# Kernel optimization log

Measured on AMD Instinct MI355X. Metric: run time of the kernel, lower is better.

Reference implementation:

```python
import jax, jax.numpy as jnp
import numpy as np

GROUPS = 32
EPS = 1e-5


def group_norm(x, gamma, beta):
    # x: [N, C, H, W]
    N, C, H, W = x.shape
    xg = x.reshape(N, GROUPS, C // GROUPS, H, W)
    mean = xg.mean(axis=(2, 3, 4), keepdims=True)
    var = xg.var(axis=(2, 3, 4), keepdims=True)
    xg = (xg - mean) * jax.lax.rsqrt(var + EPS)
    x = xg.reshape(N, C, H, W)
    return x * gamma[None, :, None, None] + beta[None, :, None, None]


def conv1x1(x, w, b):
    # x: [N, C, H, W], w: [O, C], b: [O]
    return jnp.einsum('nchw,oc->nohw', x, w) + b[None, :, None, None]


def setup_inputs() -> dict:
    key = jax.random.key(0)
    ks = jax.random.split(key, 12)
    N, C, H, W = 16, 512, 32, 32
    s = 1.0 / np.sqrt(C)
    inp = {
        'x': jax.random.normal(ks[0], (N, C, H, W), dtype=jnp.float32),
        'gamma': jnp.ones((C,), dtype=jnp.float32),
        'beta': jnp.zeros((C,), dtype=jnp.float32),
        'wq': jax.random.normal(ks[1], (C, C), dtype=jnp.float32) * s,
        'bq': jnp.zeros((C,), dtype=jnp.float32),
        'wk': jax.random.normal(ks[2], (C, C), dtype=jnp.float32) * s,
        'bk': jnp.zeros((C,), dtype=jnp.float32),
        'wv': jax.random.normal(ks[3], (C, C), dtype=jnp.float32) * s,
        'bv': jnp.zeros((C,), dtype=jnp.float32),
        'wo': jax.random.normal(ks[4], (C, C), dtype=jnp.float32) * s,
        'bo': jnp.zeros((C,), dtype=jnp.float32),
    }
    return inp


def reference(x, gamma, beta, wq, bq, wk, bk, wv, bv, wo, bo):
    N, C, H, W = x.shape
    h = group_norm(x, gamma, beta)
    q = conv1x1(h, wq, bq)  # [N, C, H, W]
    k = conv1x1(h, wk, bk)
    v = conv1x1(h, wv, bv)
    # flatten spatial dims to sequence of length S = H*W
    q = q.reshape(N, C, H * W).transpose(0, 2, 1)  # [N, S, C]
    k = k.reshape(N, C, H * W)                     # [N, C, S]
    v = v.reshape(N, C, H * W).transpose(0, 2, 1)  # [N, S, C]
    scale = C ** (-0.5)
    w = jnp.einsum('nsc,nct->nst', q, k) * scale   # [N, S, S]
    w = jax.nn.softmax(w, axis=-1)
    h = jnp.einsum('nst,ntc->nsc', w, v)           # [N, S, C]
    h = h.reshape(N, H, W, C).transpose(0, 3, 1, 2)  # [N, C, H, W]
    h = conv1x1(h, wo, bo)
    return x + h
```

## Files before the change

### kernel.cpp

```cpp
#include <hip/hip_runtime.h>

#define GROUPS 32
#define EPS 1e-5f

typedef unsigned short u16;
typedef __bf16 bf16x8 __attribute__((ext_vector_type(8)));
typedef float f32x4 __attribute__((ext_vector_type(4)));

__device__ __forceinline__ u16 f2bf(float f) {
  unsigned x = __builtin_bit_cast(unsigned, f);
  x += 0x7FFFu + ((x >> 16) & 1u);
  return (u16)(x >> 16);
}
__device__ __forceinline__ float bf2f(u16 u) {
  unsigned x = ((unsigned)u) << 16;
  return __builtin_bit_cast(float, x);
}

__device__ __forceinline__ void gload_lds16(const void* g, void* l) {
  __builtin_amdgcn_global_load_lds(
      (const __attribute__((address_space(1))) void*)g,
      (__attribute__((address_space(3))) void*)l, 16, 0, 0);
}

__global__ __launch_bounds__(256) void prep_kernel(
    const float* __restrict__ x, const float* __restrict__ gamma,
    const float* __restrict__ beta, u16* __restrict__ HT,
    const float* __restrict__ wq, const float* __restrict__ wk,
    const float* __restrict__ wv, const float* __restrict__ wo,
    const float* __restrict__ bq, const float* __restrict__ bk,
    u16* __restrict__ Wqk, u16* __restrict__ Wv, u16* __restrict__ Wo,
    float* __restrict__ bqk, float* __restrict__ lsum,
    int C, int S, int CC, int NG) {
  __shared__ float xs[16 * 1024];
  __shared__ float rs[4], rss[4];
  int b = blockIdx.x;
  int tid = threadIdx.x;

  if (b >= NG) {
    int cb = b - NG;
    if (cb < 1024) {
      int w = cb >> 8, blk = cb & 255;
      const float* src;
      u16* dst;
      switch (w) {
        case 0: src = wq; dst = Wqk; break;
        case 1: src = wk; dst = Wqk + CC; break;
        case 2: src = wv; dst = Wv; break;
        default: src = wo; dst = Wo; break;
      }
      int i = (blk * 256 + tid) * 4;
      float4 v = *(const float4*)&src[i];
      ushort4 o;
      o.x = f2bf(v.x); o.y = f2bf(v.y); o.z = f2bf(v.z); o.w = f2bf(v.w);
      *(ushort4*)&dst[i] = o;
    } else if (cb < 1028) {
      int j = (cb - 1024) * 256 + tid;
      if (j < C) bqk[j] = bq[j];
      else if (j < 2 * C) bqk[j] = bk[j - C];
    } else {
      int i = (cb - 1028) * 1024 + tid * 4;
      *(float4*)&lsum[i] = make_float4(0.f, 0.f, 0.f, 0.f);
    }
    return;
  }

  const int cpg = C / GROUPS;
  int n = b / GROUPS;
  int g = b % GROUPS;
  const float* xb = x + ((size_t)n * C + (size_t)g * cpg) * S;
  int cnt = cpg * S;
  float s = 0.f, ss = 0.f;
  for (int i = tid * 4; i < cnt; i += 256 * 4) {
    float4 v = *(const float4*)&xb[i];
    *(float4*)&xs[i] = v;
    s += v.x + v.y + v.z + v.w;
    ss += v.x * v.x + v.y * v.y + v.z * v.z + v.w * v.w;
  }
  for (int o = 32; o > 0; o >>= 1) {
    s += __shfl_xor(s, o);
    ss += __shfl_xor(ss, o);
  }
  int wave = tid >> 6, lane = tid & 63;
  if (lane == 0) { rs[wave] = s; rss[wave] = ss; }
  __syncthreads();
  float S1 = rs[0] + rs[1] + rs[2] + rs[3];
  float S2 = rss[0] + rss[1] + rss[2] + rss[3];
  float mean = S1 / (float)cnt;
  float var = S2 / (float)cnt - mean * mean;
  float rstd = rsqrtf(var + EPS);
  float gm[16], bt[16];
#pragma unroll
  for (int c = 0; c < 16; ++c) {
    float gmv = gamma[g * cpg + c] * rstd;
    gm[c] = gmv;
    bt[c] = beta[g * cpg + c] - mean * gmv;
  }
  for (int i = 0; i < S; i += 256) {
    int sp = i + tid;
    u16 outv[16];
#pragma unroll
    for (int c = 0; c < 16; ++c) {
      float h = xs[c * 1024 + sp] * gm[c] + bt[c];
      outv[c] = f2bf(h);
    }
    u16* dst = HT + ((size_t)n * S + sp) * C + g * cpg;
    *(int4*)dst = *(int4*)&outv[0];
    *(int4*)&dst[8] = *(int4*)&outv[8];
  }
}

__device__ __forceinline__ void gemm_body(
    int bid, int nblk,
    const u16* __restrict__ A, long lda, long strideA,
    const u16* __restrict__ B, long ldb, long strideB,
    void* __restrict__ Out, long ldo, long strideO, int out_fp32,
    const float* __restrict__ bias, int bias_mode,
    float scale, const float* __restrict__ residual, int K,
    int nbx, int nby, u16* lds, int epi_mode, float* epi_ptr) {
  u16* As0 = lds;
  u16* Bs0 = lds + 8192;
  u16* As1 = lds + 12288;
  u16* Bs1 = lds + 20480;

  int tid = threadIdx.x;
  int wave = tid >> 6, lane = tid & 63;
  int wr = wave >> 1, wc = wave & 1;
  int l15 = lane & 15, l4 = lane >> 4;

  int tilesPB = nbx * nby;
  int nz = nblk / tilesPB;
  int z, rem;
  if ((nz & 7) == 0) {
    int e = bid & 7, j = bid >> 3;
    z = e + 8 * (j / tilesPB);
    rem = j % tilesPB;
  } else {
    int swz = ((nblk & 7) == 0) ? (bid & 7) * (nblk >> 3) + (bid >> 3) : bid;
    z = swz / tilesPB; rem = swz % tilesPB;
  }
  int bx = rem % nbx, by = rem / nbx;

  const u16* Ab = A + (long)z * strideA + (long)by * 256 * lda;
  const u16* Bb = B + (long)z * strideB + (long)bx * 128 * ldb;

  auto STAGE = [&](u16* Ad, u16* Bd, int kt) {
#pragma unroll
    for (int i = 0; i < 2; ++i) {
      int c = i * 512 + tid;
      int l = c >> 3, p = c & 7;
      int q = p ^ (l & 7);
      int row = 2 * l + (q >> 2);
      long koff = (long)kt * 32 + (q & 3) * 8;
      int lbase = (i * 512 + wave * 64) * 8;
      gload_lds16(Ab + (long)row * lda + koff, Ad + lbase);
    }
    {
      int c = tid;
      int l = c >> 3, p = c & 7;
      int q = p ^ (l & 7);
      int row = 2 * l + (q >> 2);
      long koff = (long)kt * 32 + (q & 3) * 8;
      int lbase = (wave * 64) * 8;
      gload_lds16(Bb + (long)row * ldb + koff, Bd + lbase);
    }
  };

  f32x4 acc[4][4] = {};

  auto COMPUTE = [&](const u16* Asrc, const u16* Bsrc) {
    bf16x8 af[4], bfr[4];
#pragma unroll
    for (int m = 0; m < 4; ++m) {
      int R = wr * 64 + m * 16 + l15;
      int line = R >> 1;
      int p = ((R & 1) * 4 + l4) ^ (line & 7);
      af[m] = *(const bf16x8*)&Asrc[line * 64 + p * 8];
    }
#pragma unroll
    for (int n = 0; n < 4; ++n) {
      int R = wc * 64 + n * 16 + l15;
      int line = R >> 1;
      int p = ((R & 1) * 4 + l4) ^ (line & 7);
      bfr[n] = *(const bf16x8*)&Bsrc[line * 64 + p * 8];
    }
#pragma unroll
    for (int m = 0; m < 4; ++m)
#pragma unroll
      for (int n = 0; n < 4; ++n)
        acc[m][n] = __builtin_amdgcn_mfma_f32_16x16x32_bf16(
            af[m], bfr[n], acc[m][n], 0, 0, 0);
  };

  int NT = K >> 5;
  u16 *Ar = As0, *Br = Bs0, *Aw = As1, *Bw = Bs1;

  STAGE(Ar, Br, 0);
  asm volatile("s_waitcnt vmcnt(0)" ::: "memory");
  __builtin_amdgcn_sched_barrier(0);
  __builtin_amdgcn_s_barrier();
  __builtin_amdgcn_sched_barrier(0);

  for (int t = 0; t < NT - 1; ++t) {
    STAGE(Aw, Bw, t + 1);
    COMPUTE(Ar, Br);
    asm volatile("s_waitcnt vmcnt(0)" ::: "memory");
    __builtin_amdgcn_sched_barrier(0);
    __builtin_amdgcn_s_barrier();
    __builtin_amdgcn_sched_barrier(0);
    u16* tp;
    tp = Ar; Ar = Aw; Aw = tp;
    tp = Br; Br = Bw; Bw = tp;
  }
  COMPUTE(Ar, Br);

  long orow0 = (long)by * 256 + wr * 64;
  long ocol0 = (long)bx * 128 + wc * 64;
  long rows_pb = 256L * nby;
  long cols_pb = 128L * nbx;

  float inv4[4];
  if (epi_mode == 2) {
#pragma unroll
    for (int n = 0; n < 4; ++n)
      inv4[n] = 1.f / epi_ptr[z * cols_pb + ocol0 + n * 16 + l15];
  }
  float rowpart[4][4];
  if (epi_mode == 1) {
#pragma unroll
    for (int m = 0; m < 4; ++m)
#pragma unroll
      for (int r = 0; r < 4; ++r) rowpart[m][r] = 0.f;
  }

#pragma unroll
  for (int m = 0; m < 4; ++m) {
#pragma unroll
    for (int n = 0; n < 4; ++n) {
#pragma unroll
      for (int r = 0; r < 4; ++r) {
        long row = orow0 + m * 16 + l4 * 4 + r;
        long col = ocol0 + n * 16 + l15;
        long off = (long)z * strideO + row * ldo + col;
        float v = acc[m][n][r] * scale;
        if (epi_mode == 1) {
          u16 e = f2bf(__expf(v));
          ((u16*)Out)[off] = e;
          rowpart[m][r] += bf2f(e);
        } else {
          if (epi_mode == 2) v *= inv4[n];
          if (bias_mode == 1) v += bias[row];
          else if (bias_mode == 2) v += bias[col];
          if (residual) v += residual[off];
          if (out_fp32) ((float*)Out)[off] = v;
          else ((u16*)Out)[off] = f2bf(v);
        }
      }
    }
  }

  if (epi_mode == 1) {
#pragma unroll
    for (int m = 0; m < 4; ++m)
#pragma unroll
      for (int r = 0; r < 4; ++r) {
        float t = rowpart[m][r];
        t += __shfl_xor(t, 1);
        t += __shfl_xor(t, 2);
        t += __shfl_xor(t, 4);
        t += __shfl_xor(t, 8);
        if (l15 == 0) {
          long row = orow0 + m * 16 + l4 * 4 + r;
          atomicAdd(&epi_ptr[z * rows_pb + row], t);
        }
      }
  }
}

__global__ __launch_bounds__(512, 4) void gemm256x128_kernel(
    const u16* __restrict__ A, long lda, long strideA,
    const u16* __restrict__ B, long ldb, long strideB,
    void* __restrict__ Out, long ldo, long strideO, int out_fp32,
    const float* __restrict__ bias, int bias_mode,
    float scale, const float* __restrict__ residual, int K, int nbx, int nby,
    int epi_mode, float* epi_ptr) {
  __shared__ u16 lds[24576];
  gemm_body(blockIdx.x, gridDim.x, A, lda, strideA, B, ldb, strideB,
            Out, ldo, strideO, out_fp32, bias, bias_mode, scale, residual,
            K, nbx, nby, lds, epi_mode, epi_ptr);
}

__global__ __launch_bounds__(512, 4) void projqkv_kernel(
    const u16* __restrict__ HT, const u16* __restrict__ Wqk,
    const u16* __restrict__ Wv, u16* __restrict__ QKT, u16* __restrict__ Vb,
    const float* __restrict__ bqk, const float* __restrict__ bv,
    int nQK, int C, int S) {
  __shared__ u16 lds[24576];
  long SC = (long)S * C, S2C = (long)S * 2 * C;
  if ((int)blockIdx.x < nQK) {
    gemm_body(blockIdx.x, nQK, HT, C, SC, Wqk, C, 0, QKT, 2 * C, S2C, 0,
              bqk, 2, 1.f, nullptr, C, 2 * C / 128, S / 256, lds, 0, nullptr);
  } else {
    gemm_body(blockIdx.x - nQK, gridDim.x - nQK, Wv, C, 0, HT, C, SC,
              Vb, S, SC, 0, bv, 1, 1.f, nullptr, C, S / 128, C / 256, lds,
              0, nullptr);
  }
}

extern "C" void kernel_launch(void* const* d_in, const int* in_sizes, int n_in,
                              void* d_out, int out_size, void* d_ws, size_t ws_size,
                              hipStream_t stream) {
  const float* x = (const float*)d_in[0];
  const float* gamma = (const float*)d_in[1];
  const float* beta = (const float*)d_in[2];
  const float* wq = (const float*)d_in[3];
  const float* bq = (const float*)d_in[4];
  const float* wk = (const float*)d_in[5];
  const float* bk = (const float*)d_in[6];
  const float* wv = (const float*)d_in[7];
  const float* bv = (const float*)d_in[8];
  const float* wo = (const float*)d_in[9];
  const float* bo = (const float*)d_in[10];

  const int C = 512, S = 1024;
  const int N = in_sizes[0] / (C * S);
  const long SC = (long)S * C;
  const long S2C = (long)S * 2 * C;
  const long SS = (long)S * S;
  const int CC = C * C;

  char* ws = (char*)d_ws;
  const size_t MB = 1024 * 1024;
  u16* HT = (u16*)(ws + 0 * MB);
  u16* QKT = (u16*)(ws + 16 * MB);
  u16* Vb = (u16*)(ws + 48 * MB);
  u16* P = (u16*)(ws + 64 * MB);
  u16* Wqk = (u16*)(ws + 96 * MB);
  u16* Wv = Wqk + 2 * CC;
  u16* Wo = Wv + CC;
  float* bqk = (float*)(Wo + CC);
  float* lsum = bqk + 2 * C;
  u16* H2T = HT;

  const int NG = N * GROUPS;

  prep_kernel<<<dim3(NG + 1024 + 4 + 16), 256, 0, stream>>>(
      x, gamma, beta, HT, wq, wk, wv, wo, bq, bk, Wqk, Wv, Wo, bqk, lsum,
      C, S, CC, NG);

  const float scl = 1.0f / sqrtf((float)C);
  const int nQK = (S / 256) * (2 * C / 128) * N;
  const int nV = (C / 256) * (S / 128) * N;

  projqkv_kernel<<<dim3(nQK + nV), 512, 0, stream>>>(
      HT, Wqk, Wv, QKT, Vb, bqk, bv, nQK, C, S);
  gemm256x128_kernel<<<dim3((S / 256) * (S / 128) * N), 512, 0, stream>>>(
      QKT, 2 * C, S2C, QKT + C, 2 * C, S2C, P, S, SS, 0, nullptr, 0, scl,
      nullptr, C, S / 128, S / 256, 1, lsum);
  gemm256x128_kernel<<<dim3((S / 256) * (C / 128) * N), 512, 0, stream>>>(
      P, S, SS, Vb, S, SC, H2T, C, SC, 0, nullptr, 0, 1.f, nullptr, S,
      C / 128, S / 256, 0, nullptr);
  gemm256x128_kernel<<<dim3((C / 256) * (S / 128) * N), 512, 0, stream>>>(
      Wo, C, 0, H2T, C, SC, d_out, S, SC, 1, bo, 1, 1.f, x, C,
      S / 128, C / 256, 2, lsum);
}
```

Before: 162.3 us.

## Reassociate output projection before attention and fuse QKV projection into one GEMM

Computes V in token-major layout together with Q and K in a single projection GEMM. It then applies Wo to V first (Wo·V), running that GEMM concurrently with the QK^T score GEMM in one launch. The final GEMM multiplies the projected values by the probabilities, with residual and bias in the epilogue. This removes a launch and lets two independent GEMMs share the grid; the final GEMM's K dimension grows from C to S, and the reassociation changes where bf16 rounding happens.

Result: slower. 172.2 us (+6.1%).

```diff
diff --git a/kernel.cpp b/kernel.cpp
--- a/kernel.cpp
+++ b/kernel.cpp
@@ -29,8 +29,9 @@
     const float* __restrict__ wq, const float* __restrict__ wk,
     const float* __restrict__ wv, const float* __restrict__ wo,
     const float* __restrict__ bq, const float* __restrict__ bk,
-    u16* __restrict__ Wqk, u16* __restrict__ Wv, u16* __restrict__ Wo,
-    float* __restrict__ bqk, float* __restrict__ lsum,
+    const float* __restrict__ bv,
+    u16* __restrict__ Wqkv, u16* __restrict__ Wo,
+    float* __restrict__ bqkv, float* __restrict__ lsum,
     int C, int S, int CC, int NG) {
   __shared__ float xs[16 * 1024];
   __shared__ float rs[4], rss[4];
@@ -44,9 +45,9 @@
       const float* src;
       u16* dst;
       switch (w) {
-        case 0: src = wq; dst = Wqk; break;
-        case 1: src = wk; dst = Wqk + CC; break;
-        case 2: src = wv; dst = Wv; break;
+        case 0: src = wq; dst = Wqkv; break;
+        case 1: src = wk; dst = Wqkv + CC; break;
+        case 2: src = wv; dst = Wqkv + 2 * CC; break;
         default: src = wo; dst = Wo; break;
       }
       int i = (blk * 256 + tid) * 4;
@@ -54,12 +55,13 @@
       ushort4 o;
       o.x = f2bf(v.x); o.y = f2bf(v.y); o.z = f2bf(v.z); o.w = f2bf(v.w);
       *(ushort4*)&dst[i] = o;
-    } else if (cb < 1028) {
+    } else if (cb < 1030) {
       int j = (cb - 1024) * 256 + tid;
-      if (j < C) bqk[j] = bq[j];
-      else if (j < 2 * C) bqk[j] = bk[j - C];
+      if (j < C) bqkv[j] = bq[j];
+      else if (j < 2 * C) bqkv[j] = bk[j - C];
+      else bqkv[j] = bv[j - 2 * C];
     } else {
-      int i = (cb - 1028) * 1024 + tid * 4;
+      int i = (cb - 1030) * 1024 + tid * 4;
       *(float4*)&lsum[i] = make_float4(0.f, 0.f, 0.f, 0.f);
     }
     return;
@@ -290,20 +292,20 @@
             K, nbx, nby, lds, epi_mode, epi_ptr);
 }
 
-__global__ __launch_bounds__(512, 4) void projqkv_kernel(
-    const u16* __restrict__ HT, const u16* __restrict__ Wqk,
-    const u16* __restrict__ Wv, u16* __restrict__ QKT, u16* __restrict__ Vb,
-    const float* __restrict__ bqk, const float* __restrict__ bv,
-    int nQK, int C, int S) {
+__global__ __launch_bounds__(512, 4) void pvo_kernel(
+    const u16* __restrict__ QKVT, const u16* __restrict__ Wo,
+    u16* __restrict__ P, u16* __restrict__ VO, float* __restrict__ lsum,
+    float scl, int nP, int C, int S) {
   __shared__ u16 lds[24576];
-  long SC = (long)S * C, S2C = (long)S * 2 * C;
-  if ((int)blockIdx.x < nQK) {
-    gemm_body(blockIdx.x, nQK, HT, C, SC, Wqk, C, 0, QKT, 2 * C, S2C, 0,
-              bqk, 2, 1.f, nullptr, C, 2 * C / 128, S / 256, lds, 0, nullptr);
+  long S3C = (long)S * 3 * C, SC = (long)S * C, SS = (long)S * S;
+  if ((int)blockIdx.x < nP) {
+    gemm_body(blockIdx.x, nP, QKVT, 3 * C, S3C, QKVT + C, 3 * C, S3C,
+              P, S, SS, 0, nullptr, 0, scl, nullptr, C,
+              S / 128, S / 256, lds, 1, lsum);
   } else {
-    gemm_body(blockIdx.x - nQK, gridDim.x - nQK, Wv, C, 0, HT, C, SC,
-              Vb, S, SC, 0, bv, 1, 1.f, nullptr, C, S / 128, C / 256, lds,
-              0, nullptr);
+    gemm_body(blockIdx.x - nP, gridDim.x - nP, Wo, C, 0,
+              QKVT + 2 * C, 3 * C, S3C, VO, S, SC, 0, nullptr, 0, 1.f,
+              nullptr, C, S / 128, C / 256, lds, 0, nullptr);
   }
 }
 
@@ -325,42 +327,37 @@
   const int C = 512, S = 1024;
   const int N = in_sizes[0] / (C * S);
   const long SC = (long)S * C;
-  const long S2C = (long)S * 2 * C;
+  const long S3C = (long)S * 3 * C;
   const long SS = (long)S * S;
   const int CC = C * C;
 
   char* ws = (char*)d_ws;
   const size_t MB = 1024 * 1024;
   u16* HT = (u16*)(ws + 0 * MB);
-  u16* QKT = (u16*)(ws + 16 * MB);
-  u16* Vb = (u16*)(ws + 48 * MB);
+  u16* VO = HT;
+  u16* QKVT = (u16*)(ws + 16 * MB);
   u16* P = (u16*)(ws + 64 * MB);
-  u16* Wqk = (u16*)(ws + 96 * MB);
-  u16* Wv = Wqk + 2 * CC;
-  u16* Wo = Wv + CC;
-  float* bqk = (float*)(Wo + CC);
-  float* lsum = bqk + 2 * C;
-  u16* H2T = HT;
+  u16* Wqkv = (u16*)(ws + 96 * MB);
+  u16* Wo = Wqkv + 3 * CC;
+  float* bqkv = (float*)(Wo + CC);
+  float* lsum = bqkv + 3 * C;
 
   const int NG = N * GROUPS;
 
-  prep_kernel<<<dim3(NG + 1024 + 4 + 16), 256, 0, stream>>>(
-      x, gamma, beta, HT, wq, wk, wv, wo, bq, bk, Wqk, Wv, Wo, bqk, lsum,
+  prep_kernel<<<dim3(NG + 1024 + 6 + 16), 256, 0, stream>>>(
+      x, gamma, beta, HT, wq, wk, wv, wo, bq, bk, bv, Wqkv, Wo, bqkv, lsum,
       C, S, CC, NG);
 
   const float scl = 1.0f / sqrtf((float)C);
-  const int nQK = (S / 256) * (2 * C / 128) * N;
-  const int nV = (C / 256) * (S / 128) * N;
-
-  projqkv_kernel<<<dim3(nQK + nV), 512, 0, stream>>>(
-      HT, Wqk, Wv, QKT, Vb, bqk, bv, nQK, C, S);
-  gemm256x128_kernel<<<dim3((S / 256) * (S / 128) * N), 512, 0, stream>>>(
-      QKT, 2 * C, S2C, QKT + C, 2 * C, S2C, P, S, SS, 0, nullptr, 0, scl,
-      nullptr, C, S / 128, S / 256, 1, lsum);
-  gemm256x128_kernel<<<dim3((S / 256) * (C / 128) * N), 512, 0, stream>>>(
-      P, S, SS, Vb, S, SC, H2T, C, SC, 0, nullptr, 0, 1.f, nullptr, S,
-      C / 128, S / 256, 0, nullptr);
+  const int nP = (S / 256) * (S / 128) * N;
+  const int nVO = (C / 256) * (S / 128) * N;
+
+  gemm256x128_kernel<<<dim3((S / 256) * (3 * C / 128) * N), 512, 0, stream>>>(
+      HT, C, SC, Wqkv, C, 0, QKVT, 3 * C, S3C, 0, bqkv, 2, 1.f, nullptr, C,
+      3 * C / 128, S / 256, 0, nullptr);
+  pvo_kernel<<<dim3(nP + nVO), 512, 0, stream>>>(
+      QKVT, Wo, P, VO, lsum, scl, nP, C, S);
   gemm256x128_kernel<<<dim3((C / 256) * (S / 128) * N), 512, 0, stream>>>(
-      Wo, C, 0, H2T, C, SC, d_out, S, SC, 1, bo, 1, 1.f, x, C,
+      VO, S, SC, P, S, SS, d_out, S, SC, 1, bo, 1, 1.f, x, S,
       S / 128, C / 256, 2, lsum);
 }
```

## Fuse four GEMM launches into persistent mega-kernel with software grid barriers

Applied to the files above, without the earlier changes.

Replaces the QKV projection, QK^T, PV and output-projection launches with one persistent 512-block kernel. The stages are separated by an atomic-counter grid barrier, and the counter is reset in the prep kernel. This removes launch gaps and tail effects between kernels, but the grid is fixed at 512 blocks, so some stages run with only 256 active blocks. The barrier only works if all 512 blocks are co-resident, which is risky if occupancy drops and otherwise the kernel deadlocks.

New measurement: 296.9 us. 1.83x slower.

```diff
diff --git a/kernel.cpp b/kernel.cpp
--- a/kernel.cpp
+++ b/kernel.cpp
@@ -31,7 +31,7 @@
     const float* __restrict__ bq, const float* __restrict__ bk,
     u16* __restrict__ Wqk, u16* __restrict__ Wv, u16* __restrict__ Wo,
     float* __restrict__ bqk, float* __restrict__ lsum,
-    int C, int S, int CC, int NG) {
+    unsigned* __restrict__ bar, int C, int S, int CC, int NG) {
   __shared__ float xs[16 * 1024];
   __shared__ float rs[4], rss[4];
   int b = blockIdx.x;
@@ -58,9 +58,11 @@
       int j = (cb - 1024) * 256 + tid;
       if (j < C) bqk[j] = bq[j];
       else if (j < 2 * C) bqk[j] = bk[j - C];
-    } else {
+    } else if (cb < 1044) {
       int i = (cb - 1028) * 1024 + tid * 4;
       *(float4*)&lsum[i] = make_float4(0.f, 0.f, 0.f, 0.f);
+    } else {
+      if (tid == 0) *bar = 0u;
     }
     return;
   }
@@ -277,34 +279,54 @@
   }
 }
 
-__global__ __launch_bounds__(512, 4) void gemm256x128_kernel(
-    const u16* __restrict__ A, long lda, long strideA,
-    const u16* __restrict__ B, long ldb, long strideB,
-    void* __restrict__ Out, long ldo, long strideO, int out_fp32,
-    const float* __restrict__ bias, int bias_mode,
-    float scale, const float* __restrict__ residual, int K, int nbx, int nby,
-    int epi_mode, float* epi_ptr) {
+__device__ __forceinline__ void grid_sync(unsigned* bar, unsigned target) {
+  __syncthreads();
+  if (threadIdx.x == 0) {
+    __threadfence();
+    atomicAdd(bar, 1u);
+    while (__hip_atomic_load(bar, __ATOMIC_RELAXED,
+                             __HIP_MEMORY_SCOPE_AGENT) < target)
+      __builtin_amdgcn_s_sleep(8);
+    __threadfence();
+  }
+  __syncthreads();
+}
+
+__global__ __launch_bounds__(512, 4) void mega_kernel(
+    const u16* __restrict__ HT, const u16* __restrict__ Wqk,
+    const u16* __restrict__ Wv, const u16* __restrict__ Wo,
+    u16* __restrict__ QKT, u16* __restrict__ Vb, u16* __restrict__ P,
+    u16* __restrict__ H2T, const float* __restrict__ bqk,
+    const float* __restrict__ bv, const float* __restrict__ bo,
+    const float* __restrict__ x, float* __restrict__ Out,
+    float* __restrict__ lsum, unsigned* __restrict__ bar,
+    float scl, int C, int S) {
   __shared__ u16 lds[24576];
-  gemm_body(blockIdx.x, gridDim.x, A, lda, strideA, B, ldb, strideB,
-            Out, ldo, strideO, out_fp32, bias, bias_mode, scale, residual,
-            K, nbx, nby, lds, epi_mode, epi_ptr);
-}
-
-__global__ __launch_bounds__(512, 4) void projqkv_kernel(
-    const u16* __restrict__ HT, const u16* __restrict__ Wqk,
-    const u16* __restrict__ Wv, u16* __restrict__ QKT, u16* __restrict__ Vb,
-    const float* __restrict__ bqk, const float* __restrict__ bv,
-    int nQK, int C, int S) {
-  __shared__ u16 lds[24576];
-  long SC = (long)S * C, S2C = (long)S * 2 * C;
-  if ((int)blockIdx.x < nQK) {
-    gemm_body(blockIdx.x, nQK, HT, C, SC, Wqk, C, 0, QKT, 2 * C, S2C, 0,
-              bqk, 2, 1.f, nullptr, C, 2 * C / 128, S / 256, lds, 0, nullptr);
-  } else {
-    gemm_body(blockIdx.x - nQK, gridDim.x - nQK, Wv, C, 0, HT, C, SC,
-              Vb, S, SC, 0, bv, 1, 1.f, nullptr, C, S / 128, C / 256, lds,
-              0, nullptr);
-  }
+  long SC = (long)S * C, S2C = (long)S * 2 * C, SS = (long)S * S;
+  int b = blockIdx.x;
+  unsigned G = gridDim.x;
+
+  gemm_body(b, 512, HT, C, SC, Wqk, C, 0, QKT, 2 * C, S2C, 0, bqk, 2, 1.f,
+            nullptr, C, 2 * C / 128, S / 256, lds, 0, nullptr);
+  if (b < 256) {
+    __syncthreads();
+    gemm_body(b, 256, Wv, C, 0, HT, C, SC, Vb, S, SC, 0, bv, 1, 1.f,
+              nullptr, C, S / 128, C / 256, lds, 0, nullptr);
+  }
+  grid_sync(bar, G);
+
+  gemm_body(b, 512, QKT, 2 * C, S2C, QKT + C, 2 * C, S2C, P, S, SS, 0,
+            nullptr, 0, scl, nullptr, C, S / 128, S / 256, lds, 1, lsum);
+  grid_sync(bar, 2 * G);
+
+  if (b < 256)
+    gemm_body(b, 256, P, S, SS, Vb, S, SC, H2T, C, SC, 0, nullptr, 0, 1.f,
+              nullptr, S, C / 128, S / 256, lds, 0, nullptr);
+  grid_sync(bar, 3 * G);
+
+  if (b < 256)
+    gemm_body(b, 256, Wo, C, 0, H2T, C, SC, Out, S, SC, 1, bo, 1, 1.f,
+              x, C, S / 128, C / 256, lds, 2, lsum);
 }
 
 extern "C" void kernel_launch(void* const* d_in, const int* in_sizes, int n_in,
@@ -324,9 +346,6 @@
 
   const int C = 512, S = 1024;
   const int N = in_sizes[0] / (C * S);
-  const long SC = (long)S * C;
-  const long S2C = (long)S * 2 * C;
-  const long SS = (long)S * S;
   const int CC = C * C;
 
   char* ws = (char*)d_ws;
@@ -340,27 +359,18 @@
   u16* Wo = Wv + CC;
   float* bqk = (float*)(Wo + CC);
   float* lsum = bqk + 2 * C;
+  unsigned* bar = (unsigned*)(lsum + (size_t)N * S);
   u16* H2T = HT;
 
   const int NG = N * GROUPS;
 
-  prep_kernel<<<dim3(NG + 1024 + 4 + 16), 256, 0, stream>>>(
+  prep_kernel<<<dim3(NG + 1024 + 4 + 16 + 1), 256, 0, stream>>>(
       x, gamma, beta, HT, wq, wk, wv, wo, bq, bk, Wqk, Wv, Wo, bqk, lsum,
-      C, S, CC, NG);
+      bar, C, S, CC, NG);
 
   const float scl = 1.0f / sqrtf((float)C);
-  const int nQK = (S / 256) * (2 * C / 128) * N;
-  const int nV = (C / 256) * (S / 128) * N;
-
-  projqkv_kernel<<<dim3(nQK + nV), 512, 0, stream>>>(
-      HT, Wqk, Wv, QKT, Vb, bqk, bv, nQK, C, S);
-  gemm256x128_kernel<<<dim3((S / 256) * (S / 128) * N), 512, 0, stream>>>(
-      QKT, 2 * C, S2C, QKT + C, 2 * C, S2C, P, S, SS, 0, nullptr, 0, scl,
-      nullptr, C, S / 128, S / 256, 1, lsum);
-  gemm256x128_kernel<<<dim3((S / 256) * (C / 128) * N), 512, 0, stream>>>(
-      P, S, SS, Vb, S, SC, H2T, C, SC, 0, nullptr, 0, 1.f, nullptr, S,
-      C / 128, S / 256, 0, nullptr);
-  gemm256x128_kernel<<<dim3((C / 256) * (S / 128) * N), 512, 0, stream>>>(
-      Wo, C, 0, H2T, C, SC, d_out, S, SC, 1, bo, 1, 1.f, x, C,
-      S / 128, C / 256, 2, lsum);
-}
+
+  mega_kernel<<<dim3(512), 512, 0, stream>>>(
+      HT, Wqk, Wv, Wo, QKT, Vb, P, H2T, bqk, bv, bo, x, (float*)d_out,
+      lsum, bar, scl, C, S);
+}
```
